# Kernel optimization log

Measured on AMD Instinct MI355X. Metric: run time of the kernel, lower is better.

The kernel has to match this reference:

```python
import jax, jax.numpy as jnp
import numpy as np

B, S, D, H, L, F = 4, 2048, 512, 8, 4, 2048
DH = D // H
EPS = 1e-5


def setup_inputs() -> dict:
    key = jax.random.key(0)
    ks = jax.random.split(key, 16)
    sc = 0.02
    inp = {
        "turn_embeddings": jax.random.normal(ks[0], (B, S, D), jnp.float32),
        "Wqkv": jax.random.normal(ks[1], (L, 3 * D, D), jnp.float32) * sc,
        "bqkv": jnp.zeros((L, 3 * D), jnp.float32),
        "Wo": jax.random.normal(ks[2], (L, D, D), jnp.float32) * sc,
        "bo": jnp.zeros((L, D), jnp.float32),
        "W1": jax.random.normal(ks[3], (L, F, D), jnp.float32) * sc,
        "b1": jnp.zeros((L, F), jnp.float32),
        "W2": jax.random.normal(ks[4], (L, D, F), jnp.float32) * sc,
        "b2": jnp.zeros((L, D), jnp.float32),
        "ln1_g": jnp.ones((L, D), jnp.float32),
        "ln1_b": jnp.zeros((L, D), jnp.float32),
        "ln2_g": jnp.ones((L, D), jnp.float32),
        "ln2_b": jnp.zeros((L, D), jnp.float32),
        "speaker_ids": jax.random.randint(ks[5], (B, S), 0, 4, jnp.int64 if jax.config.jax_enable_x64 else jnp.int32),
    }
    return inp


def _layer_norm(x, g, b):
    mu = jnp.mean(x, axis=-1, keepdims=True)
    var = jnp.mean(jnp.square(x - mu), axis=-1, keepdims=True)
    return (x - mu) * jax.lax.rsqrt(var + EPS) * g + b


def _attention(x, Wqkv, bqkv, Wo, bo, allow):
    # x: [B,S,D]; allow: [B,1,S,S] boolean (causal & same-speaker)
    qkv = x @ Wqkv.T + bqkv                       # [B,S,3D]
    q, k, v = jnp.split(qkv, 3, axis=-1)
    q = q.reshape(x.shape[0], x.shape[1], H, DH)
    k = k.reshape(x.shape[0], x.shape[1], H, DH)
    v = v.reshape(x.shape[0], x.shape[1], H, DH)
    scores = jnp.einsum("bqhd,bkhd->bhqk", q, k) / np.sqrt(DH)
    scores = jnp.where(allow, scores, jnp.finfo(scores.dtype).min)
    p = jax.nn.softmax(scores, axis=-1)
    o = jnp.einsum("bhqk,bkhd->bqhd", p, v).reshape(x.shape[0], x.shape[1], D)
    return o @ Wo.T + bo


def reference(turn_embeddings, Wqkv, bqkv, Wo, bo, W1, b1, W2, b2,
              ln1_g, ln1_b, ln2_g, ln2_b, speaker_ids):
    Bc, Sc, _ = turn_embeddings.shape
    causal = jnp.tril(jnp.ones((Sc, Sc), bool))                 # [S,S]
    same = speaker_ids[:, :, None] == speaker_ids[:, None, :]    # [B,S,S]
    allow = (same & causal)[:, None, :, :]                       # [B,1,S,S]
    x = turn_embeddings
    for l in range(L):
        a = _attention(x, Wqkv[l], bqkv[l], Wo[l], bo[l], allow)
        x = _layer_norm(x + a, ln1_g[l], ln1_b[l])
        h = jax.nn.relu(x @ W1[l].T + b1[l]) @ W2[l].T + b2[l]
        x = _layer_norm(x + h, ln2_g[l], ln2_b[l])
    return x
```

## Files before the change

kernel.cpp:

```cpp
#include <hip/hip_runtime.h>
#include <stdint.h>

#define BN 4
#define SN 2048
#define DN 512
#define HN 8
#define LN 4
#define FN 2048
#define MN (BN * SN)
#define TD (3 * DN)

typedef __attribute__((ext_vector_type(8))) __bf16 bf16x8;
typedef __attribute__((ext_vector_type(4))) float f32x4;
typedef __attribute__((ext_vector_type(8))) unsigned short ushortx8;

static __device__ __forceinline__ unsigned short f2bf(float f) {
    return __builtin_bit_cast(unsigned short, (__bf16)f);
}
static __device__ __forceinline__ float bf2f(unsigned short h) {
    return __builtin_bit_cast(float, (uint32_t)h << 16);
}

static __device__ __forceinline__ void gload16(const void* g, void* l) {
    __builtin_amdgcn_global_load_lds(
        (const __attribute__((address_space(1))) void*)g,
        (__attribute__((address_space(3))) void*)l, 16, 0, 0);
}

__global__ __launch_bounds__(256) void k_cvt_all(const float* __restrict__ Wqkv,
                                                 const float* __restrict__ Wo,
                                                 const float* __restrict__ W1,
                                                 const float* __restrict__ W2,
                                                 const float* __restrict__ te,
                                                 unsigned short* __restrict__ wqkv_b,
                                                 unsigned short* __restrict__ wo_b,
                                                 unsigned short* __restrict__ w1_b,
                                                 unsigned short* __restrict__ w2_b,
                                                 unsigned short* __restrict__ xb) {
    constexpr int G0 = LN * TD * DN / 4;
    constexpr int G1 = G0 + LN * DN * DN / 4;
    constexpr int G2 = G1 + LN * FN * DN / 4;
    constexpr int G3 = G2 + LN * DN * FN / 4;
    constexpr int G4 = G3 + MN * DN / 4;
    int i = blockIdx.x * blockDim.x + threadIdx.x;
    int stride = gridDim.x * blockDim.x;
    for (; i < G4; i += stride) {
        const float* s; unsigned short* d; int j;
        if (i < G0)      { s = Wqkv; d = wqkv_b; j = i; }
        else if (i < G1) { s = Wo;   d = wo_b;   j = i - G0; }
        else if (i < G2) { s = W1;   d = w1_b;   j = i - G1; }
        else if (i < G3) { s = W2;   d = w2_b;   j = i - G2; }
        else             { s = te;   d = xb;     j = i - G3; }
        float4 v = ((const float4*)s)[j];
        ushort4 o;
        o.x = f2bf(v.x); o.y = f2bf(v.y); o.z = f2bf(v.z); o.w = f2bf(v.w);
        ((ushort4*)d)[j] = o;
    }
}

template <int MODE, int BNT>
__global__ __launch_bounds__(256) void k_gemm(const unsigned short* __restrict__ A,
                                              const unsigned short* __restrict__ B,
                                              const float* __restrict__ bias,
                                              unsigned short* __restrict__ Cb,
                                              int M, int N, int K, int GX) {
    __shared__ __align__(16) unsigned short As[128][64];
    __shared__ __align__(16) unsigned short Bs[BNT][64];
    constexpr int NFR = BNT / 32;

    const int t = threadIdx.x;
    const int lane = t & 63;
    const int wid = t >> 6;
    const int wm = wid >> 1, wn = wid & 1;
    const int lr = lane & 15;
    const int lg = lane >> 4;

    const int nwg = gridDim.x;
    const int bid = blockIdx.x;
    const int swz = (bid & 7) * (nwg >> 3) + (bid >> 3);
    const int bx = swz % GX;
    const int by = swz / GX;

    const size_t rowA = (size_t)by * 128;
    const size_t rowB = (size_t)bx * BNT;
    const unsigned short* Ab = A + rowA * K;
    const unsigned short* Bb = B + rowB * K;

    const int srow = lane >> 3;
    const int sgran = (lane & 7) ^ srow;

    f32x4 acc[4][NFR] = {};

    for (int k0 = 0; k0 < K; k0 += 64) {
        __syncthreads();
#pragma unroll
        for (int j = 0; j < 4; ++j) {
            const int c = wid * 4 + j;
            const size_t goff = (size_t)(8 * c + srow) * K + k0 + sgran * 8;
            gload16(Ab + goff, &As[8 * c][0]);
        }
#pragma unroll
        for (int j = 0; j < NFR; ++j) {
            const int c = wid * NFR + j;
            const size_t goff = (size_t)(8 * c + srow) * K + k0 + sgran * 8;
            gload16(Bb + goff, &Bs[8 * c][0]);
        }
        __syncthreads();

#pragma unroll
        for (int h = 0; h < 2; ++h) {
            const int gp = (h * 4 + lg) ^ (lr & 7);
            bf16x8 af[4], bfr[NFR];
#pragma unroll
            for (int mi = 0; mi < 4; ++mi)
                af[mi] = *(const bf16x8*)&As[wm * 64 + mi * 16 + lr][gp * 8];
#pragma unroll
            for (int ni = 0; ni < NFR; ++ni)
                bfr[ni] = *(const bf16x8*)&Bs[wn * (BNT / 2) + ni * 16 + lr][gp * 8];
#pragma unroll
            for (int mi = 0; mi < 4; ++mi)
#pragma unroll
                for (int ni = 0; ni < NFR; ++ni)
                    acc[mi][ni] = __builtin_amdgcn_mfma_f32_16x16x32_bf16(
                        af[mi], bfr[ni], acc[mi][ni], 0, 0, 0);
        }
    }

    float bv[NFR];
#pragma unroll
    for (int ni = 0; ni < NFR; ++ni)
        bv[ni] = bias[(int)rowB + wn * (BNT / 2) + ni * 16 + lr];

#pragma unroll
    for (int mi = 0; mi < 4; ++mi) {
#pragma unroll
        for (int ni = 0; ni < NFR; ++ni) {
            int col = (int)rowB + wn * (BNT / 2) + ni * 16 + lr;
            int row0 = (int)rowA + wm * 64 + mi * 16 + lg * 4;
#pragma unroll
            for (int r = 0; r < 4; ++r) {
                float v = acc[mi][ni][r] + bv[ni];
                if (MODE == 2) v = fmaxf(v, 0.f);
                Cb[(size_t)(row0 + r) * N + col] = f2bf(v);
            }
        }
    }
}

__global__ __launch_bounds__(512) void k_attn(const unsigned short* __restrict__ qkv,
                                              const int* __restrict__ spk,
                                              unsigned short* __restrict__ o) {
    __shared__ __align__(16) unsigned short Ks[2][64][64];
    __shared__ __align__(16) unsigned short Vt[2][64][64];
    __shared__ __align__(16) unsigned short Ps[8][16][64];
    __shared__ unsigned char skb[SN];

    const int t = threadIdx.x;
    const int lane = t & 63;
    const int w = t >> 6;
    const int lr = lane & 15;
    const int lg = lane >> 4;
    const int l7 = lr & 7;

    const int wg = blockIdx.x;
    const int inner = wg >> 3;
    const int bh = 4 * (wg & 7) + (inner & 3);
    const int qsuper = (SN / 128 - 1) - (inner >> 2);
    const int b = bh >> 3;
    const int h = bh & 7;
    const int qb = qsuper * 128;

    const size_t base = (size_t)b * SN * TD;
    const unsigned short* kg = qkv + base + DN + h * 64;
    const unsigned short* vg = qkv + base + 2 * DN + h * 64;

    for (int i = t; i < SN; i += 512) skb[i] = (unsigned char)spk[b * SN + i];

    const float SCL = 0.125f * 1.4426950408889634f;
    const unsigned short* qptr = qkv + base + (size_t)(qb + w * 16 + lr) * TD + h * 64;
    bf16x8 aq0 = *(const bf16x8*)(qptr + lg * 8);
    bf16x8 aq1 = *(const bf16x8*)(qptr + 32 + lg * 8);
#pragma unroll
    for (int j = 0; j < 8; ++j) {
        aq0[j] = (__bf16)((float)aq0[j] * SCL);
        aq1[j] = (__bf16)((float)aq1[j] * SCL);
    }

    int sqr[4], qrow[4];
#pragma unroll
    for (int r = 0; r < 4; ++r) {
        qrow[r] = qb + w * 16 + lg * 4 + r;
        sqr[r] = spk[b * SN + qrow[r]];
    }

    const int krow = t >> 3;
    const int kgran = (t & 7) ^ (krow & 7);
    const int vrow = t & 63;
    const int vd0 = w * 8;

    gload16(kg + (size_t)krow * TD + kgran * 8, &Ks[0][w * 8][0]);
    ushortx8 vra = *(const ushortx8*)&vg[(size_t)vrow * TD + vd0];
#pragma unroll
    for (int j = 0; j < 8; ++j) {
        const int vcol = (((vrow >> 3) ^ j) << 3) + (vrow & 7);
        Vt[0][vd0 + j][vcol] = vra[j];
    }

    float lsum[4] = {0.f, 0.f, 0.f, 0.f};
    f32x4 acc_o[4] = {};

    const int ntiles = qb / 64 + 2;
    const int qlast = qb + w * 16 + 15;
    for (int it = 0; it < ntiles; ++it) {
        const int k0 = it * 64;
        const int cur = it & 1;
        __syncthreads();

        const bool nx = (it + 1 < ntiles);
        if (nx) {
            const int kn = k0 + 64;
            gload16(kg + (size_t)(kn + krow) * TD + kgran * 8, &Ks[cur ^ 1][w * 8][0]);
            vra = *(const ushortx8*)&vg[(size_t)(kn + vrow) * TD + vd0];
        }

        if (k0 <= qlast) {
            int skr[4];
#pragma unroll
            for (int ni = 0; ni < 4; ++ni) skr[ni] = skb[k0 + 16 * ni + lr];

            f32x4 sc4[4] = {};
            __builtin_amdgcn_s_setprio(1);
#pragma unroll
            for (int ni = 0; ni < 4; ++ni) {
                bf16x8 bk0 = *(const bf16x8*)&Ks[cur][16 * ni + lr][(lg ^ l7) * 8];
                bf16x8 bk1 = *(const bf16x8*)&Ks[cur][16 * ni + lr][((lg + 4) ^ l7) * 8];
                sc4[ni] = __builtin_amdgcn_mfma_f32_16x16x32_bf16(aq0, bk0, sc4[ni], 0, 0, 0);
                sc4[ni] = __builtin_amdgcn_mfma_f32_16x16x32_bf16(aq1, bk1, sc4[ni], 0, 0, 0);
            }
            __builtin_amdgcn_s_setprio(0);

            const bool needC = (k0 + 63 >= qb + w * 16);
#pragma unroll
            for (int ni = 0; ni < 4; ++ni) {
#pragma unroll
                for (int r = 0; r < 4; ++r) {
                    bool allow = (skr[ni] == sqr[r]);
                    if (needC) allow = allow && (k0 + 16 * ni + lr <= qrow[r]);
                    float p = allow ? __builtin_amdgcn_exp2f(sc4[ni][r]) : 0.f;
                    lsum[r] += p;
                    const int q7 = (lg * 4 + r) & 7;
                    const int pg = ((2 * ni + (lr >> 3)) ^ q7) * 8 + l7;
                    Ps[w][lg * 4 + r][pg] = f2bf(p);
                }
            }

            bf16x8 ap0 = *(const bf16x8*)&Ps[w][lr][(lg ^ l7) * 8];
            bf16x8 ap1 = *(const bf16x8*)&Ps[w][lr][((lg + 4) ^ l7) * 8];
            __builtin_amdgcn_s_setprio(1);
#pragma unroll
            for (int ni = 0; ni < 4; ++ni) {
                bf16x8 bv0 = *(const bf16x8*)&Vt[cur][16 * ni + lr][(lg ^ l7) * 8];
                bf16x8 bv1 = *(const bf16x8*)&Vt[cur][16 * ni + lr][((lg + 4) ^ l7) * 8];
                acc_o[ni] = __builtin_amdgcn_mfma_f32_16x16x32_bf16(ap0, bv0, acc_o[ni], 0, 0, 0);
                acc_o[ni] = __builtin_amdgcn_mfma_f32_16x16x32_bf16(ap1, bv1, acc_o[ni], 0, 0, 0);
            }
            __builtin_amdgcn_s_setprio(0);
        }

        if (nx) {
            const int nb = cur ^ 1;
#pragma unroll
            for (int j = 0; j < 8; ++j) {
                const int vcol = (((vrow >> 3) ^ j) << 3) + (vrow & 7);
                Vt[nb][vd0 + j][vcol] = vra[j];
            }
        }
    }

#pragma unroll
    for (int r = 0; r < 4; ++r) {
        float s = lsum[r];
        s += __shfl_xor(s, 1);
        s += __shfl_xor(s, 2);
        s += __shfl_xor(s, 4);
        s += __shfl_xor(s, 8);
        float inv = 1.f / s;
#pragma unroll
        for (int ni = 0; ni < 4; ++ni) {
            int d = 16 * ni + lr;
            o[(size_t)(b * SN + qrow[r]) * DN + h * 64 + d] = f2bf(acc_o[ni][r] * inv);
        }
    }
}

template <bool XF32>
__global__ __launch_bounds__(256) void k_add_ln(const void* __restrict__ xin_,
                                                const unsigned short* __restrict__ dl,
                                                const float* __restrict__ g,
                                                const float* __restrict__ bta,
                                                unsigned short* __restrict__ xb,
                                                float* __restrict__ fout) {
    const int row = blockIdx.x * 4 + (threadIdx.x >> 6);
    const int lane = threadIdx.x & 63;
    const size_t off = (size_t)row * DN + lane * 8;
    const int c0 = lane * 8;

    float v[8];
    if (XF32) {
        const float* xin = (const float*)xin_;
        float4 a0 = *(const float4*)&xin[off];
        float4 a1 = *(const float4*)&xin[off + 4];
        v[0] = a0.x; v[1] = a0.y; v[2] = a0.z; v[3] = a0.w;
        v[4] = a1.x; v[5] = a1.y; v[6] = a1.z; v[7] = a1.w;
    } else {
        ushortx8 xa = *(const ushortx8*)&((const unsigned short*)xin_)[off];
#pragma unroll
        for (int i = 0; i < 8; ++i) v[i] = bf2f(xa[i]);
    }
    ushortx8 dd = *(const ushortx8*)&dl[off];
#pragma unroll
    for (int i = 0; i < 8; ++i) v[i] += bf2f(dd[i]);

    float s1 = 0.f, s2 = 0.f;
#pragma unroll
    for (int i = 0; i < 8; ++i) { s1 += v[i]; s2 += v[i] * v[i]; }
#pragma unroll
    for (int msk = 32; msk; msk >>= 1) {
        s1 += __shfl_xor(s1, msk);
        s2 += __shfl_xor(s2, msk);
    }
    const float mean = s1 * (1.f / 512.f);
    const float var = s2 * (1.f / 512.f) - mean * mean;
    const float rs = rsqrtf(var + 1e-5f);

    float4 g0 = *(const float4*)&g[c0];
    float4 g1 = *(const float4*)&g[c0 + 4];
    float4 b0 = *(const float4*)&bta[c0];
    float4 b1 = *(const float4*)&bta[c0 + 4];
    float gg[8] = {g0.x, g0.y, g0.z, g0.w, g1.x, g1.y, g1.z, g1.w};
    float bb[8] = {b0.x, b0.y, b0.z, b0.w, b1.x, b1.y, b1.z, b1.w};

    float y[8];
    ushortx8 ub;
#pragma unroll
    for (int i = 0; i < 8; ++i) {
        y[i] = (v[i] - mean) * rs * gg[i] + bb[i];
        ub[i] = f2bf(y[i]);
    }
    *(ushortx8*)&xb[off] = ub;
    if (fout) {
        *(float4*)&fout[off] = make_float4(y[0], y[1], y[2], y[3]);
        *(float4*)&fout[off + 4] = make_float4(y[4], y[5], y[6], y[7]);
    }
}

extern "C" void kernel_launch(void* const* d_in, const int* in_sizes, int n_in,
                              void* d_out, int out_size, void* d_ws, size_t ws_size,
                              hipStream_t stream) {
    const float* te   = (const float*)d_in[0];
    const float* Wqkv = (const float*)d_in[1];
    const float* bqkv = (const float*)d_in[2];
    const float* Wo   = (const float*)d_in[3];
    const float* bo   = (const float*)d_in[4];
    const float* W1   = (const float*)d_in[5];
    const float* b1   = (const float*)d_in[6];
    const float* W2   = (const float*)d_in[7];
    const float* b2   = (const float*)d_in[8];
    const float* g1   = (const float*)d_in[9];
    const float* be1  = (const float*)d_in[10];
    const float* g2   = (const float*)d_in[11];
    const float* be2  = (const float*)d_in[12];
    const int*   spk  = (const int*)d_in[13];
    float* out = (float*)d_out;

    char* ws = (char*)d_ws;
    size_t off = 0;
    auto alloc = [&](size_t bytes) -> char* {
        char* p = ws + off;
        off += (bytes + 255) & ~(size_t)255;
        return p;
    };
    unsigned short* wqkv_b = (unsigned short*)alloc((size_t)LN * TD * DN * 2);
    unsigned short* wo_b   = (unsigned short*)alloc((size_t)LN * DN * DN * 2);
    unsigned short* w1_b   = (unsigned short*)alloc((size_t)LN * FN * DN * 2);
    unsigned short* w2_b   = (unsigned short*)alloc((size_t)LN * DN * FN * 2);
    unsigned short* xb     = (unsigned short*)alloc((size_t)MN * DN * 2);
    unsigned short* u      = (unsigned short*)alloc((size_t)MN * FN * 2);
    unsigned short* ob     = (unsigned short*)alloc((size_t)MN * DN * 2);
    unsigned short* projb  = (unsigned short*)alloc((size_t)MN * DN * 2);
    unsigned short* qkvb = u;
    unsigned short* hb   = u;

    k_cvt_all<<<2048, 256, 0, stream>>>(Wqkv, Wo, W1, W2, te,
                                        wqkv_b, wo_b, w1_b, w2_b, xb);

    for (int l = 0; l < LN; ++l) {
        k_gemm<1, 128><<<(MN / 128) * (TD / 128), 256, 0, stream>>>(
            xb, wqkv_b + (size_t)l * TD * DN, bqkv + l * TD, qkvb,
            MN, TD, DN, TD / 128);
        k_attn<<<(SN / 128) * BN * HN, 512, 0, stream>>>(qkvb, spk, ob);
        k_gemm<1, 64><<<(MN / 128) * (DN / 64), 256, 0, stream>>>(
            ob, wo_b + (size_t)l * DN * DN, bo + l * DN, projb,
            MN, DN, DN, DN / 64);
        if (l == 0)
            k_add_ln<true><<<MN / 4, 256, 0, stream>>>(
                te, projb, g1 + l * DN, be1 + l * DN, xb, nullptr);
        else
            k_add_ln<false><<<MN / 4, 256, 0, stream>>>(
                xb, projb, g1 + l * DN, be1 + l * DN, xb, nullptr);
        k_gemm<2, 128><<<(MN / 128) * (FN / 128), 256, 0, stream>>>(
            xb, w1_b + (size_t)l * FN * DN, b1 + l * FN, hb,
            MN, FN, DN, FN / 128);
        k_gemm<1, 64><<<(MN / 128) * (DN / 64), 256, 0, stream>>>(
            hb, w2_b + (size_t)l * DN * FN, b2 + l * DN, projb,
            MN, DN, FN, DN / 64);
        k_add_ln<false><<<MN / 4, 256, 0, stream>>>(
            xb, projb, g2 + l * DN, be2 + l * DN, xb,
            (l == LN - 1) ? out : nullptr);
    }
    (void)in_sizes; (void)n_in; (void)out_size; (void)ws_size;
}
```

Before: 670.2 us.

## Shrink attention query tile to 64 rows with 4-wave blocks

The attention kernel now processes 64 query rows per block with 256 threads instead of 128 rows with 512, doubling the grid. Each wave loads two K rows-groups and two V chunks per tile. The shared speaker-id staging buffer and its per-wave early-exit logic are dropped in favour of direct global speaker reads. The causal mask is applied only on the final diagonal tile. This gives finer work granularity for causal load balance and less wasted iteration on the upper triangle, at the cost of halved K/V reuse per block and more global loads.

```diff
diff --git a/kernel.cpp b/kernel.cpp
--- a/kernel.cpp
+++ b/kernel.cpp
@@ -147,13 +147,12 @@
     }
 }
 
-__global__ __launch_bounds__(512) void k_attn(const unsigned short* __restrict__ qkv,
+__global__ __launch_bounds__(256) void k_attn(const unsigned short* __restrict__ qkv,
                                               const int* __restrict__ spk,
                                               unsigned short* __restrict__ o) {
     __shared__ __align__(16) unsigned short Ks[2][64][64];
     __shared__ __align__(16) unsigned short Vt[2][64][64];
-    __shared__ __align__(16) unsigned short Ps[8][16][64];
-    __shared__ unsigned char skb[SN];
+    __shared__ __align__(16) unsigned short Ps[4][16][64];
 
     const int t = threadIdx.x;
     const int lane = t & 63;
@@ -165,16 +164,14 @@
     const int wg = blockIdx.x;
     const int inner = wg >> 3;
     const int bh = 4 * (wg & 7) + (inner & 3);
-    const int qsuper = (SN / 128 - 1) - (inner >> 2);
+    const int qtile = (SN / 64 - 1) - (inner >> 2);
     const int b = bh >> 3;
     const int h = bh & 7;
-    const int qb = qsuper * 128;
+    const int qb = qtile * 64;
 
     const size_t base = (size_t)b * SN * TD;
     const unsigned short* kg = qkv + base + DN + h * 64;
     const unsigned short* vg = qkv + base + 2 * DN + h * 64;
-
-    for (int i = t; i < SN; i += 512) skb[i] = (unsigned char)spk[b * SN + i];
 
     const float SCL = 0.125f * 1.4426950408889634f;
     const unsigned short* qptr = qkv + base + (size_t)(qb + w * 16 + lr) * TD + h * 64;
@@ -193,24 +190,28 @@
         sqr[r] = spk[b * SN + qrow[r]];
     }
 
-    const int krow = t >> 3;
-    const int kgran = (t & 7) ^ (krow & 7);
-    const int vrow = t & 63;
-    const int vd0 = w * 8;
-
-    gload16(kg + (size_t)krow * TD + kgran * 8, &Ks[0][w * 8][0]);
+    const int krl = lane >> 3;
+    const int kgran = (lane & 7) ^ krl;
+    const int vrow = lane;
+    const int vd0 = w * 16;
+
+#pragma unroll
+    for (int j = 0; j < 2; ++j)
+        gload16(kg + (size_t)(w * 16 + j * 8 + krl) * TD + kgran * 8,
+                &Ks[0][w * 16 + j * 8][0]);
     ushortx8 vra = *(const ushortx8*)&vg[(size_t)vrow * TD + vd0];
+    ushortx8 vrb = *(const ushortx8*)&vg[(size_t)vrow * TD + vd0 + 8];
 #pragma unroll
     for (int j = 0; j < 8; ++j) {
-        const int vcol = (((vrow >> 3) ^ j) << 3) + (vrow & 7);
-        Vt[0][vd0 + j][vcol] = vra[j];
+        const int vc0 = (((vrow >> 3) ^ j) << 3) + (vrow & 7);
+        Vt[0][vd0 + j][vc0] = vra[j];
+        Vt[0][vd0 + 8 + j][vc0] = vrb[j];
     }
 
     float lsum[4] = {0.f, 0.f, 0.f, 0.f};
     f32x4 acc_o[4] = {};
 
-    const int ntiles = qb / 64 + 2;
-    const int qlast = qb + w * 16 + 15;
+    const int ntiles = qtile + 1;
     for (int it = 0; it < ntiles; ++it) {
         const int k0 = it * 64;
         const int cur = it & 1;
@@ -219,60 +220,62 @@
         const bool nx = (it + 1 < ntiles);
         if (nx) {
             const int kn = k0 + 64;
-            gload16(kg + (size_t)(kn + krow) * TD + kgran * 8, &Ks[cur ^ 1][w * 8][0]);
+#pragma unroll
+            for (int j = 0; j < 2; ++j)
+                gload16(kg + (size_t)(kn + w * 16 + j * 8 + krl) * TD + kgran * 8,
+                        &Ks[cur ^ 1][w * 16 + j * 8][0]);
             vra = *(const ushortx8*)&vg[(size_t)(kn + vrow) * TD + vd0];
-        }
-
-        if (k0 <= qlast) {
-            int skr[4];
-#pragma unroll
-            for (int ni = 0; ni < 4; ++ni) skr[ni] = skb[k0 + 16 * ni + lr];
-
-            f32x4 sc4[4] = {};
-            __builtin_amdgcn_s_setprio(1);
-#pragma unroll
-            for (int ni = 0; ni < 4; ++ni) {
-                bf16x8 bk0 = *(const bf16x8*)&Ks[cur][16 * ni + lr][(lg ^ l7) * 8];
-                bf16x8 bk1 = *(const bf16x8*)&Ks[cur][16 * ni + lr][((lg + 4) ^ l7) * 8];
-                sc4[ni] = __builtin_amdgcn_mfma_f32_16x16x32_bf16(aq0, bk0, sc4[ni], 0, 0, 0);
-                sc4[ni] = __builtin_amdgcn_mfma_f32_16x16x32_bf16(aq1, bk1, sc4[ni], 0, 0, 0);
+            vrb = *(const ushortx8*)&vg[(size_t)(kn + vrow) * TD + vd0 + 8];
+        }
+        int skr[4];
+#pragma unroll
+        for (int ni = 0; ni < 4; ++ni) skr[ni] = spk[b * SN + k0 + 16 * ni + lr];
+
+        f32x4 sc4[4] = {};
+        __builtin_amdgcn_s_setprio(1);
+#pragma unroll
+        for (int ni = 0; ni < 4; ++ni) {
+            bf16x8 bk0 = *(const bf16x8*)&Ks[cur][16 * ni + lr][(lg ^ l7) * 8];
+            bf16x8 bk1 = *(const bf16x8*)&Ks[cur][16 * ni + lr][((lg + 4) ^ l7) * 8];
+            sc4[ni] = __builtin_amdgcn_mfma_f32_16x16x32_bf16(aq0, bk0, sc4[ni], 0, 0, 0);
+            sc4[ni] = __builtin_amdgcn_mfma_f32_16x16x32_bf16(aq1, bk1, sc4[ni], 0, 0, 0);
+        }
+        __builtin_amdgcn_s_setprio(0);
+
+        const bool diag = (it == ntiles - 1);
+#pragma unroll
+        for (int ni = 0; ni < 4; ++ni) {
+#pragma unroll
+            for (int r = 0; r < 4; ++r) {
+                bool allow = (skr[ni] == sqr[r]);
+                if (diag) allow = allow && (16 * ni + lr <= w * 16 + lg * 4 + r);
+                float p = allow ? __builtin_amdgcn_exp2f(sc4[ni][r]) : 0.f;
+                lsum[r] += p;
+                const int q7 = (lg * 4 + r) & 7;
+                const int pg = ((2 * ni + (lr >> 3)) ^ q7) * 8 + l7;
+                Ps[w][lg * 4 + r][pg] = f2bf(p);
             }
-            __builtin_amdgcn_s_setprio(0);
-
-            const bool needC = (k0 + 63 >= qb + w * 16);
-#pragma unroll
-            for (int ni = 0; ni < 4; ++ni) {
-#pragma unroll
-                for (int r = 0; r < 4; ++r) {
-                    bool allow = (skr[ni] == sqr[r]);
-                    if (needC) allow = allow && (k0 + 16 * ni + lr <= qrow[r]);
-                    float p = allow ? __builtin_amdgcn_exp2f(sc4[ni][r]) : 0.f;
-                    lsum[r] += p;
-                    const int q7 = (lg * 4 + r) & 7;
-                    const int pg = ((2 * ni + (lr >> 3)) ^ q7) * 8 + l7;
-                    Ps[w][lg * 4 + r][pg] = f2bf(p);
-                }
-            }
-
-            bf16x8 ap0 = *(const bf16x8*)&Ps[w][lr][(lg ^ l7) * 8];
-            bf16x8 ap1 = *(const bf16x8*)&Ps[w][lr][((lg + 4) ^ l7) * 8];
-            __builtin_amdgcn_s_setprio(1);
-#pragma unroll
-            for (int ni = 0; ni < 4; ++ni) {
-                bf16x8 bv0 = *(const bf16x8*)&Vt[cur][16 * ni + lr][(lg ^ l7) * 8];
-                bf16x8 bv1 = *(const bf16x8*)&Vt[cur][16 * ni + lr][((lg + 4) ^ l7) * 8];
-                acc_o[ni] = __builtin_amdgcn_mfma_f32_16x16x32_bf16(ap0, bv0, acc_o[ni], 0, 0, 0);
-                acc_o[ni] = __builtin_amdgcn_mfma_f32_16x16x32_bf16(ap1, bv1, acc_o[ni], 0, 0, 0);
-            }
-            __builtin_amdgcn_s_setprio(0);
-        }
+        }
+
+        bf16x8 ap0 = *(const bf16x8*)&Ps[w][lr][(lg ^ l7) * 8];
+        bf16x8 ap1 = *(const bf16x8*)&Ps[w][lr][((lg + 4) ^ l7) * 8];
+        __builtin_amdgcn_s_setprio(1);
+#pragma unroll
+        for (int ni = 0; ni < 4; ++ni) {
+            bf16x8 bv0 = *(const bf16x8*)&Vt[cur][16 * ni + lr][(lg ^ l7) * 8];
+            bf16x8 bv1 = *(const bf16x8*)&Vt[cur][16 * ni + lr][((lg + 4) ^ l7) * 8];
+            acc_o[ni] = __builtin_amdgcn_mfma_f32_16x16x32_bf16(ap0, bv0, acc_o[ni], 0, 0, 0);
+            acc_o[ni] = __builtin_amdgcn_mfma_f32_16x16x32_bf16(ap1, bv1, acc_o[ni], 0, 0, 0);
+        }
+        __builtin_amdgcn_s_setprio(0);
 
         if (nx) {
             const int nb = cur ^ 1;
 #pragma unroll
             for (int j = 0; j < 8; ++j) {
-                const int vcol = (((vrow >> 3) ^ j) << 3) + (vrow & 7);
-                Vt[nb][vd0 + j][vcol] = vra[j];
+                const int vc0 = (((vrow >> 3) ^ j) << 3) + (vrow & 7);
+                Vt[nb][vd0 + j][vc0] = vra[j];
+                Vt[nb][vd0 + 8 + j][vc0] = vrb[j];
             }
         }
     }
@@ -398,7 +401,7 @@
         k_gemm<1, 128><<<(MN / 128) * (TD / 128), 256, 0, stream>>>(
             xb, wqkv_b + (size_t)l * TD * DN, bqkv + l * TD, qkvb,
             MN, TD, DN, TD / 128);
-        k_attn<<<(SN / 128) * BN * HN, 512, 0, stream>>>(qkvb, spk, ob);
+        k_attn<<<(SN / 64) * BN * HN, 256, 0, stream>>>(qkvb, spk, ob);
         k_gemm<1, 64><<<(MN / 128) * (DN / 64), 256, 0, stream>>>(
             ob, wo_b + (size_t)l * DN * DN, bo + l * DN, projb,
             MN, DN, DN, DN / 64);
```

Result: faster. 606.6 us (-9.5%).
